# Kernel optimization log

Measured on AMD Instinct MI355X. Metric: run time of the kernel, lower is better.

Reference implementation:

```python
import jax, jax.numpy as jnp
import numpy as np

N_NODES = 100000
N_EDGES = 3200000
IN_F = 256
OUT_F = 128


def setup_inputs() -> dict:
    key = jax.random.key(0)
    k1, k2, k3, k4, k5, k6 = jax.random.split(key, 6)
    x = jax.random.normal(k1, (N_NODES, IN_F), dtype=jnp.float32)
    edge_row = jax.random.randint(k2, (N_EDGES,), 0, N_NODES, dtype=jnp.int32)
    edge_col = jax.random.randint(k3, (N_EDGES,), 0, N_NODES, dtype=jnp.int32)
    edge_val = jax.random.uniform(k4, (N_EDGES,), dtype=jnp.float32)
    # xavier_uniform with relu gain, as in reset_parameters
    gain = float(np.sqrt(2.0))
    bound = gain * float(np.sqrt(6.0 / (IN_F + OUT_F)))
    w = jax.random.uniform(k5, (IN_F, OUT_F), minval=-bound, maxval=bound, dtype=jnp.float32)
    std = 1.0 / float(np.sqrt(OUT_F))
    bias = jax.random.uniform(k6, (OUT_F,), minval=-std, maxval=std, dtype=jnp.float32)
    return {"x": x, "edge_row": edge_row, "edge_col": edge_col,
            "edge_val": edge_val, "w": w, "bias": bias}


def reference(x, edge_row, edge_col, edge_val, w, bias):
    # h = x @ w : dense feature transform [N, out]
    h = jnp.matmul(x, w)
    # spmm(adj, h): out[r] = sum_e adj_val[e] * h[c[e]] for edges e with row r
    msgs = edge_val[:, None] * h[edge_col]  # [E, out]
    agg = jax.ops.segment_sum(msgs, edge_row, num_segments=N_NODES)
    return agg + bias
```

## Files before the change

kernel.cpp:

```cpp
#include <hip/hip_runtime.h>
#include <hip/hip_bf16.h>

#define N_NODES 100000
#define N_EDGES 3200000
#define IN_F 256
#define OUT_F 128

#define RPB 128
#define NBIN 782
#define NBC  896
#define CHUNK 3572
#define GEMM_BLOCKS 782
#define BPTC 4
#define CAP 4608

typedef __attribute__((ext_vector_type(8))) short bf16x8;
typedef __attribute__((ext_vector_type(4))) float f32x4;

union U4BF { uint4 u; bf16x8 v; };

__device__ inline unsigned short f2bf(float f) {
    return __bfloat16_as_ushort(__float2bfloat16(f));
}
__device__ inline unsigned pk2(float a, float b) {
    unsigned la = __bfloat16_as_ushort(__float2bfloat16(a));
    unsigned lb = __bfloat16_as_ushort(__float2bfloat16(b));
    return la | (lb << 16);
}

__global__ __launch_bounds__(256) void conv_w_kernel(
    const float* __restrict__ w, uint4* __restrict__ wbfF)
{
    int tid = blockIdx.x * 256 + threadIdx.x;
    int ks = tid >> 9;
    int fn = (tid >> 6) & 7;
    int l  = tid & 63;
    int c  = fn * 16 + (l & 15);
    int k0 = ks * 32 + (l >> 4) * 8;
    const float* wp = w + (size_t)k0 * OUT_F + c;
    uint4 u;
    u.x = pk2(wp[0 * OUT_F], wp[1 * OUT_F]);
    u.y = pk2(wp[2 * OUT_F], wp[3 * OUT_F]);
    u.z = pk2(wp[4 * OUT_F], wp[5 * OUT_F]);
    u.w = pk2(wp[6 * OUT_F], wp[7 * OUT_F]);
    wbfF[tid] = u;
}

__global__ __launch_bounds__(256) void gemm_hist_kernel(
    const float* __restrict__ x, const uint4* __restrict__ wbfF,
    unsigned short* __restrict__ h,
    const int* __restrict__ erow, int* __restrict__ cntmat)
{
    __shared__ __align__(16) char smem[65536];
    const int t = threadIdx.x;

    if (blockIdx.x < GEMM_BLOCKS) {
        uint4* bsh = (uint4*)smem;
        const int lane = t & 63;
        const int wid  = t >> 6;
        const int brow = blockIdx.x * 128;
        const int ln   = lane & 15;
        const int kb   = lane >> 4;

#pragma unroll
        for (int i = 0; i < 16; ++i) bsh[i * 256 + t] = wbfF[i * 256 + t];

        int r0 = brow + wid * 32 + ln;
        int r1 = r0 + 16;
        const float* a0p = x + (size_t)(r0 < N_NODES ? r0 : N_NODES - 1) * IN_F;
        const float* a1p = x + (size_t)(r1 < N_NODES ? r1 : N_NODES - 1) * IN_F;

        f32x4 acc[2][8] = {};
        __syncthreads();

#pragma unroll
        for (int ks = 0; ks < 8; ++ks) {
            const int k = ks * 32 + kb * 8;
            U4BF a0, a1;
            {
                float4 p = *(const float4*)(a0p + k);
                float4 q = *(const float4*)(a0p + k + 4);
                a0.u.x = pk2(p.x, p.y); a0.u.y = pk2(p.z, p.w);
                a0.u.z = pk2(q.x, q.y); a0.u.w = pk2(q.z, q.w);
            }
            {
                float4 p = *(const float4*)(a1p + k);
                float4 q = *(const float4*)(a1p + k + 4);
                a1.u.x = pk2(p.x, p.y); a1.u.y = pk2(p.z, p.w);
                a1.u.z = pk2(q.x, q.y); a1.u.w = pk2(q.z, q.w);
            }
            U4BF b[8];
#pragma unroll
            for (int fn = 0; fn < 8; ++fn)
                b[fn].u = bsh[(ks * 8 + fn) * 64 + lane];
#pragma unroll
            for (int fn = 0; fn < 8; ++fn) {
                acc[0][fn] = __builtin_amdgcn_mfma_f32_16x16x32_bf16(
                    a0.v, b[fn].v, acc[0][fn], 0, 0, 0);
                acc[1][fn] = __builtin_amdgcn_mfma_f32_16x16x32_bf16(
                    a1.v, b[fn].v, acc[1][fn], 0, 0, 0);
            }
        }

#pragma unroll
        for (int fm = 0; fm < 2; ++fm) {
#pragma unroll
            for (int r = 0; r < 4; ++r) {
                int grow = brow + wid * 32 + fm * 16 + (lane >> 4) * 4 + r;
                if (grow < N_NODES) {
                    unsigned short* dst = h + (size_t)grow * OUT_F + ln;
#pragma unroll
                    for (int fn = 0; fn < 8; ++fn)
                        dst[fn * 16] = f2bf(acc[fm][fn][r]);
                }
            }
        }
    } else {
        int* lhist = (int*)smem;
        const int b = blockIdx.x - GEMM_BLOCKS;
        for (int i = t; i < NBIN; i += 256) lhist[i] = 0;
        __syncthreads();

        const int base = b * CHUNK;
        const int end  = min(base + CHUNK, N_EDGES);
        for (int i = base + t * 4; i < end; i += 1024) {
            int4 r = *(const int4*)(erow + i);
            atomicAdd(&lhist[r.x >> 7], 1);
            atomicAdd(&lhist[r.y >> 7], 1);
            atomicAdd(&lhist[r.z >> 7], 1);
            atomicAdd(&lhist[r.w >> 7], 1);
        }
        __syncthreads();

        int* dst = cntmat + (size_t)b * NBIN;
        for (int j = t; j < NBIN; j += 256) dst[j] = lhist[j];
    }
}

__global__ __launch_bounds__(256) void pass_b_kernel(
    const int* __restrict__ cntmat, int* __restrict__ blockbase,
    int* __restrict__ tot)
{
    __shared__ int sh[256];
    const int t = threadIdx.x;
    const int j = blockIdx.x;
    int c[4];
    int ps = 0;
#pragma unroll
    for (int i = 0; i < 4; ++i) {
        int bb = 4 * t + i;
        c[i] = (bb < NBC) ? cntmat[(size_t)bb * NBIN + j] : 0;
        ps += c[i];
    }
    sh[t] = ps;
    __syncthreads();
    for (int off = 1; off < 256; off <<= 1) {
        int add = (t >= off) ? sh[t - off] : 0;
        __syncthreads();
        sh[t] += add;
        __syncthreads();
    }
    int excl = sh[t] - ps;
#pragma unroll
    for (int i = 0; i < 4; ++i) {
        int bb = 4 * t + i;
        if (bb < NBC) { blockbase[(size_t)bb * NBIN + j] = excl; excl += c[i]; }
    }
    if (t == 255) tot[j] = sh[255];
}

__global__ __launch_bounds__(512) void pass_b2_kernel(
    const int* __restrict__ tot, int* __restrict__ bucket_base)
{
    __shared__ int sh[512];
    const int t = threadIdx.x;
    const int i0 = 2 * t, i1 = 2 * t + 1;
    int v0 = (i0 < NBIN) ? tot[i0] : 0;
    int v1 = (i1 < NBIN) ? tot[i1] : 0;
    int ps = v0 + v1;
    sh[t] = ps;
    __syncthreads();
    for (int off = 1; off < 512; off <<= 1) {
        int add = (t >= off) ? sh[t - off] : 0;
        __syncthreads();
        sh[t] += add;
        __syncthreads();
    }
    int excl = sh[t] - ps;
    if (i0 <= NBIN) bucket_base[i0] = excl;
    if (i1 <= NBIN) bucket_base[i1] = excl + v0;
}

__global__ __launch_bounds__(256) void pass_c_kernel(
    const int* __restrict__ erow, const int* __restrict__ ecol,
    const float* __restrict__ eval_, const int* __restrict__ cntmat,
    const int* __restrict__ blockbase, const int* __restrict__ bucket_base,
    int2* __restrict__ tmp)
{
    __shared__ int2 skv[CHUNK];
    __shared__ unsigned short sbin[CHUNK];
    __shared__ int  cur[NBIN];
    __shared__ int  sdel[NBIN];
    __shared__ int  sscan[256];

    const int t = threadIdx.x;
    const int b = blockIdx.x;

    int c[BPTC];
    int ps = 0;
#pragma unroll
    for (int i = 0; i < BPTC; ++i) {
        int bin = t * BPTC + i;
        c[i] = (bin < NBIN) ? cntmat[(size_t)b * NBIN + bin] : 0;
        ps += c[i];
    }
    sscan[t] = ps;
    __syncthreads();
    for (int off = 1; off < 256; off <<= 1) {
        int add = (t >= off) ? sscan[t - off] : 0;
        __syncthreads();
        sscan[t] += add;
        __syncthreads();
    }
    int excl = sscan[t] - ps;
#pragma unroll
    for (int i = 0; i < BPTC; ++i) {
        int bin = t * BPTC + i;
        if (bin < NBIN) {
            cur[bin]  = excl;
            sdel[bin] = bucket_base[bin] + blockbase[(size_t)b * NBIN + bin] - excl;
            excl += c[i];
        }
    }
    __syncthreads();

    const int base = b * CHUNK;
    const int end  = min(base + CHUNK, N_EDGES);
    for (int i = base + t * 4; i < end; i += 1024) {
        int4   r = *(const int4*)(erow + i);
        int4   cc = *(const int4*)(ecol + i);
        float4 v = *(const float4*)(eval_ + i);
        int bin, pos;
        bin = r.x >> 7; pos = atomicAdd(&cur[bin], 1);
        skv[pos] = make_int2(cc.x | ((r.x & 127) << 17), __float_as_int(v.x));
        sbin[pos] = (unsigned short)bin;
        bin = r.y >> 7; pos = atomicAdd(&cur[bin], 1);
        skv[pos] = make_int2(cc.y | ((r.y & 127) << 17), __float_as_int(v.y));
        sbin[pos] = (unsigned short)bin;
        bin = r.z >> 7; pos = atomicAdd(&cur[bin], 1);
        skv[pos] = make_int2(cc.z | ((r.z & 127) << 17), __float_as_int(v.z));
        sbin[pos] = (unsigned short)bin;
        bin = r.w >> 7; pos = atomicAdd(&cur[bin], 1);
        skv[pos] = make_int2(cc.w | ((r.w & 127) << 17), __float_as_int(v.w));
        sbin[pos] = (unsigned short)bin;
    }
    __syncthreads();

    const int n = end - base;
    for (int i = t; i < n; i += 256) {
        int2 kv = skv[i];
        tmp[sdel[sbin[i]] + i] = kv;
    }
}

__global__ __launch_bounds__(512) void fused_da_kernel(
    const int2* __restrict__ tmp, const int* __restrict__ bucket_base,
    const unsigned* __restrict__ h2, const float* __restrict__ bias,
    float* __restrict__ out)
{
    __shared__ int2 skv[CAP];
    __shared__ int  srow[RPB];
    __shared__ int  scnt[RPB];
    __shared__ int  cursor[RPB];

    const int t    = threadIdx.x;
    const int lane = t & 63;
    const int w    = t >> 6;
    const int j    = blockIdx.x;
    const int base = bucket_base[j];
    int n = bucket_base[j + 1] - base;
    if (n > CAP) n = CAP;

    if (t < RPB) cursor[t] = 0;
    __syncthreads();
    for (int i = t; i < n; i += 512)
        atomicAdd(&cursor[tmp[base + i].x >> 17], 1);
    __syncthreads();
    if (t < RPB) { scnt[t] = cursor[t]; srow[t] = cursor[t]; }
    __syncthreads();
    for (int off = 1; off < RPB; off <<= 1) {
        int add = (t >= off && t < RPB) ? srow[t - off] : 0;
        __syncthreads();
        if (t < RPB) srow[t] += add;
        __syncthreads();
    }
    if (t < RPB) { int ex = srow[t] - scnt[t]; srow[t] = ex; cursor[t] = ex; }
    __syncthreads();

    for (int i = t; i < n; i += 512) {
        int2 p = tmp[base + i];
        int rl = p.x >> 17;
        int pos = atomicAdd(&cursor[rl], 1);
        skv[pos] = make_int2(p.x & 0x1FFFF, p.y);
    }
    __syncthreads();

    const unsigned* hb = h2 + lane;
#pragma unroll 1
    for (int rr = w * 16; rr < w * 16 + 16; ++rr) {
        int gr = j * RPB + rr;
        if (gr >= N_NODES) break;
        int s = srow[rr];
        int end = s + scnt[rr];
        float ax = 0.f, ay = 0.f;

        int e = s;
        for (; e + 7 < end; e += 8) {
            int2 p0 = skv[e];
            int2 p1 = skv[e + 1];
            int2 p2 = skv[e + 2];
            int2 p3 = skv[e + 3];
            int2 p4 = skv[e + 4];
            int2 p5 = skv[e + 5];
            int2 p6 = skv[e + 6];
            int2 p7 = skv[e + 7];
            unsigned u0 = hb[(size_t)p0.x << 6];
            unsigned u1 = hb[(size_t)p1.x << 6];
            unsigned u2 = hb[(size_t)p2.x << 6];
            unsigned u3 = hb[(size_t)p3.x << 6];
            unsigned u4 = hb[(size_t)p4.x << 6];
            unsigned u5 = hb[(size_t)p5.x << 6];
            unsigned u6 = hb[(size_t)p6.x << 6];
            unsigned u7 = hb[(size_t)p7.x << 6];
            float v0 = __int_as_float(p0.y), v1 = __int_as_float(p1.y);
            float v2 = __int_as_float(p2.y), v3 = __int_as_float(p3.y);
            float v4 = __int_as_float(p4.y), v5 = __int_as_float(p5.y);
            float v6 = __int_as_float(p6.y), v7 = __int_as_float(p7.y);
            ax = fmaf(v0, __uint_as_float(u0 << 16), ax);
            ay = fmaf(v0, __uint_as_float(u0 & 0xFFFF0000u), ay);
            ax = fmaf(v1, __uint_as_float(u1 << 16), ax);
            ay = fmaf(v1, __uint_as_float(u1 & 0xFFFF0000u), ay);
            ax = fmaf(v2, __uint_as_float(u2 << 16), ax);
            ay = fmaf(v2, __uint_as_float(u2 & 0xFFFF0000u), ay);
            ax = fmaf(v3, __uint_as_float(u3 << 16), ax);
            ay = fmaf(v3, __uint_as_float(u3 & 0xFFFF0000u), ay);
            ax = fmaf(v4, __uint_as_float(u4 << 16), ax);
            ay = fmaf(v4, __uint_as_float(u4 & 0xFFFF0000u), ay);
            ax = fmaf(v5, __uint_as_float(u5 << 16), ax);
            ay = fmaf(v5, __uint_as_float(u5 & 0xFFFF0000u), ay);
            ax = fmaf(v6, __uint_as_float(u6 << 16), ax);
            ay = fmaf(v6, __uint_as_float(u6 & 0xFFFF0000u), ay);
            ax = fmaf(v7, __uint_as_float(u7 << 16), ax);
            ay = fmaf(v7, __uint_as_float(u7 & 0xFFFF0000u), ay);
        }
        for (; e < end; ++e) {
            int2 p0 = skv[e];
            unsigned u0 = hb[(size_t)p0.x << 6];
            float v0 = __int_as_float(p0.y);
            ax = fmaf(v0, __uint_as_float(u0 << 16), ax);
            ay = fmaf(v0, __uint_as_float(u0 & 0xFFFF0000u), ay);
        }

        float2 bb = *(const float2*)(bias + lane * 2);
        *(float2*)(out + (size_t)gr * OUT_F + lane * 2) =
            make_float2(ax + bb.x, ay + bb.y);
    }
}

extern "C" void kernel_launch(void* const* d_in, const int* in_sizes, int n_in,
                              void* d_out, int out_size, void* d_ws, size_t ws_size,
                              hipStream_t stream)
{
    const float* x     = (const float*)d_in[0];
    const int*   erow  = (const int*)d_in[1];
    const int*   ecol  = (const int*)d_in[2];
    const float* eval_ = (const float*)d_in[3];
    const float* w     = (const float*)d_in[4];
    const float* bias  = (const float*)d_in[5];
    float*       out   = (float*)d_out;

    char* ws = (char*)d_ws;
    unsigned short* h           = (unsigned short*)(ws);
    int2*           tmp         = (int2*)(ws + 25600000);
    int*            cntmat      = (int*)(ws + 51200000);
    int*            blockbase   = (int*)(ws + 54002688);
    int*            tot         = (int*)(ws + 56805376);
    int*            bucket_base = (int*)(ws + 56812000);
    uint4*          wbfF        = (uint4*)(ws + 56816000);

    hipLaunchKernelGGL(conv_w_kernel, dim3(16), dim3(256), 0, stream, w, wbfF);

    hipLaunchKernelGGL(gemm_hist_kernel, dim3(GEMM_BLOCKS + NBC), dim3(256), 0, stream,
                       x, wbfF, h, erow, cntmat);

    hipLaunchKernelGGL(pass_b_kernel, dim3(NBIN), dim3(256), 0, stream,
                       cntmat, blockbase, tot);
    hipLaunchKernelGGL(pass_b2_kernel, dim3(1), dim3(512), 0, stream, tot, bucket_base);

    hipLaunchKernelGGL(pass_c_kernel, dim3(NBC), dim3(256), 0, stream,
                       erow, ecol, eval_, cntmat, blockbase, bucket_base, tmp);

    hipLaunchKernelGGL(fused_da_kernel, dim3(NBIN), dim3(512), 0, stream,
                       tmp, bucket_base, (const unsigned*)h, bias, out);
}
```

Measured before the change: 197.5 us.

## Regroup kernels: fuse weight conversion with histogram, overlap GEMM with scatter pass

Weight bf16 conversion now shares a launch with the edge histogram, and the dense GEMM now shares a launch with the bucket scatter (pass C) rather than with the histogram. This removes one kernel launch and lets the heavier scatter overlap the GEMM. Separately, the aggregation kernel caches each bucket's edges in shared memory on the first read and sorts 16-bit indices instead of rewriting int2 pairs, so the global tmp array is read once instead of twice. The cost is an extra indirection through shared memory in the inner gather loop and more shared memory per block.

After: 236.4 us. 1.2x slower.

```diff
diff --git a/kernel.cpp b/kernel.cpp
--- a/kernel.cpp
+++ b/kernel.cpp
@@ -11,6 +11,7 @@
 #define NBC  896
 #define CHUNK 3572
 #define GEMM_BLOCKS 782
+#define CONV_BLOCKS 16
 #define BPTC 4
 #define CAP 4608
 
@@ -28,28 +29,109 @@
     return la | (lb << 16);
 }
 
-__global__ __launch_bounds__(256) void conv_w_kernel(
-    const float* __restrict__ w, uint4* __restrict__ wbfF)
-{
-    int tid = blockIdx.x * 256 + threadIdx.x;
-    int ks = tid >> 9;
-    int fn = (tid >> 6) & 7;
-    int l  = tid & 63;
-    int c  = fn * 16 + (l & 15);
-    int k0 = ks * 32 + (l >> 4) * 8;
-    const float* wp = w + (size_t)k0 * OUT_F + c;
-    uint4 u;
-    u.x = pk2(wp[0 * OUT_F], wp[1 * OUT_F]);
-    u.y = pk2(wp[2 * OUT_F], wp[3 * OUT_F]);
-    u.z = pk2(wp[4 * OUT_F], wp[5 * OUT_F]);
-    u.w = pk2(wp[6 * OUT_F], wp[7 * OUT_F]);
-    wbfF[tid] = u;
-}
-
-__global__ __launch_bounds__(256) void gemm_hist_kernel(
+__global__ __launch_bounds__(256) void conv_hist_kernel(
+    const float* __restrict__ w, uint4* __restrict__ wbfF,
+    const int* __restrict__ erow, int* __restrict__ cntmat)
+{
+    __shared__ int lhist[NBIN];
+    const int t = threadIdx.x;
+
+    if (blockIdx.x < CONV_BLOCKS) {
+        int tid = blockIdx.x * 256 + t;
+        int ks = tid >> 9;
+        int fn = (tid >> 6) & 7;
+        int l  = tid & 63;
+        int c  = fn * 16 + (l & 15);
+        int k0 = ks * 32 + (l >> 4) * 8;
+        const float* wp = w + (size_t)k0 * OUT_F + c;
+        uint4 u;
+        u.x = pk2(wp[0 * OUT_F], wp[1 * OUT_F]);
+        u.y = pk2(wp[2 * OUT_F], wp[3 * OUT_F]);
+        u.z = pk2(wp[4 * OUT_F], wp[5 * OUT_F]);
+        u.w = pk2(wp[6 * OUT_F], wp[7 * OUT_F]);
+        wbfF[tid] = u;
+    } else {
+        const int b = blockIdx.x - CONV_BLOCKS;
+        for (int i = t; i < NBIN; i += 256) lhist[i] = 0;
+        __syncthreads();
+
+        const int base = b * CHUNK;
+        const int end  = min(base + CHUNK, N_EDGES);
+        for (int i = base + t * 4; i < end; i += 1024) {
+            int4 r = *(const int4*)(erow + i);
+            atomicAdd(&lhist[r.x >> 7], 1);
+            atomicAdd(&lhist[r.y >> 7], 1);
+            atomicAdd(&lhist[r.z >> 7], 1);
+            atomicAdd(&lhist[r.w >> 7], 1);
+        }
+        __syncthreads();
+
+        int* dst = cntmat + (size_t)b * NBIN;
+        for (int j = t; j < NBIN; j += 256) dst[j] = lhist[j];
+    }
+}
+
+__global__ __launch_bounds__(256) void pass_b_kernel(
+    const int* __restrict__ cntmat, int* __restrict__ blockbase,
+    int* __restrict__ tot)
+{
+    __shared__ int sh[256];
+    const int t = threadIdx.x;
+    const int j = blockIdx.x;
+    int c[4];
+    int ps = 0;
+#pragma unroll
+    for (int i = 0; i < 4; ++i) {
+        int bb = 4 * t + i;
+        c[i] = (bb < NBC) ? cntmat[(size_t)bb * NBIN + j] : 0;
+        ps += c[i];
+    }
+    sh[t] = ps;
+    __syncthreads();
+    for (int off = 1; off < 256; off <<= 1) {
+        int add = (t >= off) ? sh[t - off] : 0;
+        __syncthreads();
+        sh[t] += add;
+        __syncthreads();
+    }
+    int excl = sh[t] - ps;
+#pragma unroll
+    for (int i = 0; i < 4; ++i) {
+        int bb = 4 * t + i;
+        if (bb < NBC) { blockbase[(size_t)bb * NBIN + j] = excl; excl += c[i]; }
+    }
+    if (t == 255) tot[j] = sh[255];
+}
+
+__global__ __launch_bounds__(512) void pass_b2_kernel(
+    const int* __restrict__ tot, int* __restrict__ bucket_base)
+{
+    __shared__ int sh[512];
+    const int t = threadIdx.x;
+    const int i0 = 2 * t, i1 = 2 * t + 1;
+    int v0 = (i0 < NBIN) ? tot[i0] : 0;
+    int v1 = (i1 < NBIN) ? tot[i1] : 0;
+    int ps = v0 + v1;
+    sh[t] = ps;
+    __syncthreads();
+    for (int off = 1; off < 512; off <<= 1) {
+        int add = (t >= off) ? sh[t - off] : 0;
+        __syncthreads();
+        sh[t] += add;
+        __syncthreads();
+    }
+    int excl = sh[t] - ps;
+    if (i0 <= NBIN) bucket_base[i0] = excl;
+    if (i1 <= NBIN) bucket_base[i1] = excl + v0;
+}
+
+__global__ __launch_bounds__(256) void gemm_passc_kernel(
     const float* __restrict__ x, const uint4* __restrict__ wbfF,
     unsigned short* __restrict__ h,
-    const int* __restrict__ erow, int* __restrict__ cntmat)
+    const int* __restrict__ erow, const int* __restrict__ ecol,
+    const float* __restrict__ eval_, const int* __restrict__ cntmat,
+    const int* __restrict__ blockbase, const int* __restrict__ bucket_base,
+    int2* __restrict__ tmp)
 {
     __shared__ __align__(16) char smem[65536];
     const int t = threadIdx.x;
@@ -116,150 +198,69 @@
             }
         }
     } else {
-        int* lhist = (int*)smem;
+        int2*           skv   = (int2*)(smem);
+        unsigned short* sbin  = (unsigned short*)(smem + 28576);
+        int*            cur   = (int*)(smem + 35720);
+        int*            sdel  = (int*)(smem + 38848);
+        int*            sscan = (int*)(smem + 41976);
+
         const int b = blockIdx.x - GEMM_BLOCKS;
-        for (int i = t; i < NBIN; i += 256) lhist[i] = 0;
+
+        int c[BPTC];
+        int ps = 0;
+#pragma unroll
+        for (int i = 0; i < BPTC; ++i) {
+            int bin = t * BPTC + i;
+            c[i] = (bin < NBIN) ? cntmat[(size_t)b * NBIN + bin] : 0;
+            ps += c[i];
+        }
+        sscan[t] = ps;
+        __syncthreads();
+        for (int off = 1; off < 256; off <<= 1) {
+            int add = (t >= off) ? sscan[t - off] : 0;
+            __syncthreads();
+            sscan[t] += add;
+            __syncthreads();
+        }
+        int excl = sscan[t] - ps;
+#pragma unroll
+        for (int i = 0; i < BPTC; ++i) {
+            int bin = t * BPTC + i;
+            if (bin < NBIN) {
+                cur[bin]  = excl;
+                sdel[bin] = bucket_base[bin] + blockbase[(size_t)b * NBIN + bin] - excl;
+                excl += c[i];
+            }
+        }
         __syncthreads();
 
         const int base = b * CHUNK;
         const int end  = min(base + CHUNK, N_EDGES);
         for (int i = base + t * 4; i < end; i += 1024) {
-            int4 r = *(const int4*)(erow + i);
-            atomicAdd(&lhist[r.x >> 7], 1);
-            atomicAdd(&lhist[r.y >> 7], 1);
-            atomicAdd(&lhist[r.z >> 7], 1);
-            atomicAdd(&lhist[r.w >> 7], 1);
-        }
-        __syncthreads();
-
-        int* dst = cntmat + (size_t)b * NBIN;
-        for (int j = t; j < NBIN; j += 256) dst[j] = lhist[j];
-    }
-}
-
-__global__ __launch_bounds__(256) void pass_b_kernel(
-    const int* __restrict__ cntmat, int* __restrict__ blockbase,
-    int* __restrict__ tot)
-{
-    __shared__ int sh[256];
-    const int t = threadIdx.x;
-    const int j = blockIdx.x;
-    int c[4];
-    int ps = 0;
-#pragma unroll
-    for (int i = 0; i < 4; ++i) {
-        int bb = 4 * t + i;
-        c[i] = (bb < NBC) ? cntmat[(size_t)bb * NBIN + j] : 0;
-        ps += c[i];
-    }
-    sh[t] = ps;
-    __syncthreads();
-    for (int off = 1; off < 256; off <<= 1) {
-        int add = (t >= off) ? sh[t - off] : 0;
-        __syncthreads();
-        sh[t] += add;
-        __syncthreads();
-    }
-    int excl = sh[t] - ps;
-#pragma unroll
-    for (int i = 0; i < 4; ++i) {
-        int bb = 4 * t + i;
-        if (bb < NBC) { blockbase[(size_t)bb * NBIN + j] = excl; excl += c[i]; }
-    }
-    if (t == 255) tot[j] = sh[255];
-}
-
-__global__ __launch_bounds__(512) void pass_b2_kernel(
-    const int* __restrict__ tot, int* __restrict__ bucket_base)
-{
-    __shared__ int sh[512];
-    const int t = threadIdx.x;
-    const int i0 = 2 * t, i1 = 2 * t + 1;
-    int v0 = (i0 < NBIN) ? tot[i0] : 0;
-    int v1 = (i1 < NBIN) ? tot[i1] : 0;
-    int ps = v0 + v1;
-    sh[t] = ps;
-    __syncthreads();
-    for (int off = 1; off < 512; off <<= 1) {
-        int add = (t >= off) ? sh[t - off] : 0;
-        __syncthreads();
-        sh[t] += add;
-        __syncthreads();
-    }
-    int excl = sh[t] - ps;
-    if (i0 <= NBIN) bucket_base[i0] = excl;
-    if (i1 <= NBIN) bucket_base[i1] = excl + v0;
-}
-
-__global__ __launch_bounds__(256) void pass_c_kernel(
-    const int* __restrict__ erow, const int* __restrict__ ecol,
-    const float* __restrict__ eval_, const int* __restrict__ cntmat,
-    const int* __restrict__ blockbase, const int* __restrict__ bucket_base,
-    int2* __restrict__ tmp)
-{
-    __shared__ int2 skv[CHUNK];
-    __shared__ unsigned short sbin[CHUNK];
-    __shared__ int  cur[NBIN];
-    __shared__ int  sdel[NBIN];
-    __shared__ int  sscan[256];
-
-    const int t = threadIdx.x;
-    const int b = blockIdx.x;
-
-    int c[BPTC];
-    int ps = 0;
-#pragma unroll
-    for (int i = 0; i < BPTC; ++i) {
-        int bin = t * BPTC + i;
-        c[i] = (bin < NBIN) ? cntmat[(size_t)b * NBIN + bin] : 0;
-        ps += c[i];
-    }
-    sscan[t] = ps;
-    __syncthreads();
-    for (int off = 1; off < 256; off <<= 1) {
-        int add = (t >= off) ? sscan[t - off] : 0;
-        __syncthreads();
-        sscan[t] += add;
-        __syncthreads();
-    }
-    int excl = sscan[t] - ps;
-#pragma unroll
-    for (int i = 0; i < BPTC; ++i) {
-        int bin = t * BPTC + i;
-        if (bin < NBIN) {
-            cur[bin]  = excl;
-            sdel[bin] = bucket_base[bin] + blockbase[(size_t)b * NBIN + bin] - excl;
-            excl += c[i];
-        }
-    }
-    __syncthreads();
-
-    const int base = b * CHUNK;
-    const int end  = min(base + CHUNK, N_EDGES);
-    for (int i = base + t * 4; i < end; i += 1024) {
-        int4   r = *(const int4*)(erow + i);
-        int4   cc = *(const int4*)(ecol + i);
-        float4 v = *(const float4*)(eval_ + i);
-        int bin, pos;
-        bin = r.x >> 7; pos = atomicAdd(&cur[bin], 1);
-        skv[pos] = make_int2(cc.x | ((r.x & 127) << 17), __float_as_int(v.x));
-        sbin[pos] = (unsigned short)bin;
-        bin = r.y >> 7; pos = atomicAdd(&cur[bin], 1);
-        skv[pos] = make_int2(cc.y | ((r.y & 127) << 17), __float_as_int(v.y));
-        sbin[pos] = (unsigned short)bin;
-        bin = r.z >> 7; pos = atomicAdd(&cur[bin], 1);
-        skv[pos] = make_int2(cc.z | ((r.z & 127) << 17), __float_as_int(v.z));
-        sbin[pos] = (unsigned short)bin;
-        bin = r.w >> 7; pos = atomicAdd(&cur[bin], 1);
-        skv[pos] = make_int2(cc.w | ((r.w & 127) << 17), __float_as_int(v.w));
-        sbin[pos] = (unsigned short)bin;
-    }
-    __syncthreads();
-
-    const int n = end - base;
-    for (int i = t; i < n; i += 256) {
-        int2 kv = skv[i];
-        tmp[sdel[sbin[i]] + i] = kv;
+            int4   r = *(const int4*)(erow + i);
+            int4   cc = *(const int4*)(ecol + i);
+            float4 v = *(const float4*)(eval_ + i);
+            int bin, pos;
+            bin = r.x >> 7; pos = atomicAdd(&cur[bin], 1);
+            skv[pos] = make_int2(cc.x | ((r.x & 127) << 17), __float_as_int(v.x));
+            sbin[pos] = (unsigned short)bin;
+            bin = r.y >> 7; pos = atomicAdd(&cur[bin], 1);
+            skv[pos] = make_int2(cc.y | ((r.y & 127) << 17), __float_as_int(v.y));
+            sbin[pos] = (unsigned short)bin;
+            bin = r.z >> 7; pos = atomicAdd(&cur[bin], 1);
+            skv[pos] = make_int2(cc.z | ((r.z & 127) << 17), __float_as_int(v.z));
+            sbin[pos] = (unsigned short)bin;
+            bin = r.w >> 7; pos = atomicAdd(&cur[bin], 1);
+            skv[pos] = make_int2(cc.w | ((r.w & 127) << 17), __float_as_int(v.w));
+            sbin[pos] = (unsigned short)bin;
+        }
+        __syncthreads();
+
+        const int n = end - base;
+        for (int i = t; i < n; i += 256) {
+            int2 kv = skv[i];
+            tmp[sdel[sbin[i]] + i] = kv;
+        }
     }
 }
 
@@ -269,6 +270,7 @@
     float* __restrict__ out)
 {
     __shared__ int2 skv[CAP];
+    __shared__ unsigned short sidx[CAP];
     __shared__ int  srow[RPB];
     __shared__ int  scnt[RPB];
     __shared__ int  cursor[RPB];
@@ -283,9 +285,13 @@
 
     if (t < RPB) cursor[t] = 0;
     __syncthreads();
-    for (int i = t; i < n; i += 512)
-        atomicAdd(&cursor[tmp[base + i].x >> 17], 1);
-    __syncthreads();
+    for (int i = t; i < n; i += 512) {
+        int2 p = tmp[base + i];
+        skv[i] = p;
+        atomicAdd(&cursor[p.x >> 17], 1);
+    }
+    __syncthreads();
+
     if (t < RPB) { scnt[t] = cursor[t]; srow[t] = cursor[t]; }
     __syncthreads();
     for (int off = 1; off < RPB; off <<= 1) {
@@ -298,10 +304,9 @@
     __syncthreads();
 
     for (int i = t; i < n; i += 512) {
-        int2 p = tmp[base + i];
-        int rl = p.x >> 17;
+        int rl = skv[i].x >> 17;
         int pos = atomicAdd(&cursor[rl], 1);
-        skv[pos] = make_int2(p.x & 0x1FFFF, p.y);
+        sidx[pos] = (unsigned short)i;
     }
     __syncthreads();
 
@@ -316,22 +321,22 @@
 
         int e = s;
         for (; e + 7 < end; e += 8) {
-            int2 p0 = skv[e];
-            int2 p1 = skv[e + 1];
-            int2 p2 = skv[e + 2];
-            int2 p3 = skv[e + 3];
-            int2 p4 = skv[e + 4];
-            int2 p5 = skv[e + 5];
-            int2 p6 = skv[e + 6];
-            int2 p7 = skv[e + 7];
-            unsigned u0 = hb[(size_t)p0.x << 6];
-            unsigned u1 = hb[(size_t)p1.x << 6];
-            unsigned u2 = hb[(size_t)p2.x << 6];
-            unsigned u3 = hb[(size_t)p3.x << 6];
-            unsigned u4 = hb[(size_t)p4.x << 6];
-            unsigned u5 = hb[(size_t)p5.x << 6];
-            unsigned u6 = hb[(size_t)p6.x << 6];
-            unsigned u7 = hb[(size_t)p7.x << 6];
+            int2 p0 = skv[sidx[e]];
+            int2 p1 = skv[sidx[e + 1]];
+            int2 p2 = skv[sidx[e + 2]];
+            int2 p3 = skv[sidx[e + 3]];
+            int2 p4 = skv[sidx[e + 4]];
+            int2 p5 = skv[sidx[e + 5]];
+            int2 p6 = skv[sidx[e + 6]];
+            int2 p7 = skv[sidx[e + 7]];
+            unsigned u0 = hb[(size_t)(p0.x & 0x1FFFF) << 6];
+            unsigned u1 = hb[(size_t)(p1.x & 0x1FFFF) << 6];
+            unsigned u2 = hb[(size_t)(p2.x & 0x1FFFF) << 6];
+            unsigned u3 = hb[(size_t)(p3.x & 0x1FFFF) << 6];
+            unsigned u4 = hb[(size_t)(p4.x & 0x1FFFF) << 6];
+            unsigned u5 = hb[(size_t)(p5.x & 0x1FFFF) << 6];
+            unsigned u6 = hb[(size_t)(p6.x & 0x1FFFF) << 6];
+            unsigned u7 = hb[(size_t)(p7.x & 0x1FFFF) << 6];
             float v0 = __int_as_float(p0.y), v1 = __int_as_float(p1.y);
             float v2 = __int_as_float(p2.y), v3 = __int_as_float(p3.y);
             float v4 = __int_as_float(p4.y), v5 = __int_as_float(p5.y);
@@ -354,8 +359,8 @@
             ay = fmaf(v7, __uint_as_float(u7 & 0xFFFF0000u), ay);
         }
         for (; e < end; ++e) {
-            int2 p0 = skv[e];
-            unsigned u0 = hb[(size_t)p0.x << 6];
+            int2 p0 = skv[sidx[e]];
+            unsigned u0 = hb[(size_t)(p0.x & 0x1FFFF) << 6];
             float v0 = __int_as_float(p0.y);
             ax = fmaf(v0, __uint_as_float(u0 << 16), ax);
             ay = fmaf(v0, __uint_as_float(u0 & 0xFFFF0000u), ay);
@@ -388,17 +393,16 @@
     int*            bucket_base = (int*)(ws + 56812000);
     uint4*          wbfF        = (uint4*)(ws + 56816000);
 
-    hipLaunchKernelGGL(conv_w_kernel, dim3(16), dim3(256), 0, stream, w, wbfF);
-
-    hipLaunchKernelGGL(gemm_hist_kernel, dim3(GEMM_BLOCKS + NBC), dim3(256), 0, stream,
-                       x, wbfF, h, erow, cntmat);
+    hipLaunchKernelGGL(conv_hist_kernel, dim3(CONV_BLOCKS + NBC), dim3(256), 0, stream,
+                       w, wbfF, erow, cntmat);
 
     hipLaunchKernelGGL(pass_b_kernel, dim3(NBIN), dim3(256), 0, stream,
                        cntmat, blockbase, tot);
     hipLaunchKernelGGL(pass_b2_kernel, dim3(1), dim3(512), 0, stream, tot, bucket_base);
 
-    hipLaunchKernelGGL(pass_c_kernel, dim3(NBC), dim3(256), 0, stream,
-                       erow, ecol, eval_, cntmat, blockbase, bucket_base, tmp);
+    hipLaunchKernelGGL(gemm_passc_kernel, dim3(GEMM_BLOCKS + NBC), dim3(256), 0, stream,
+                       x, wbfF, h, erow, ecol, eval_, cntmat, blockbase,
+                       bucket_base, tmp);
 
     hipLaunchKernelGGL(fused_da_kernel, dim3(NBIN), dim3(512), 0, stream,
                        tmp, bucket_base, (const unsigned*)h, bias, out);
```

## Co-schedule GEMM with edge scatter pass instead of with histogram

Applied to the files above, without the earlier changes.

Moves the weight conversion into the histogram kernel and pairs the dense GEMM blocks with the heavier pass_c scatter blocks in one launch, so the GEMM overlaps the bucket scatter rather than the light histogram. The intent is to hide the costlier scatter pass behind GEMM compute and drop one kernel launch. The shared-memory carve-up for the scatter path is now manual offsets within the 64KB buffer.

New measurement: 191.6 us. 1.03x faster.

```diff
diff --git a/kernel.cpp b/kernel.cpp
--- a/kernel.cpp
+++ b/kernel.cpp
@@ -11,6 +11,7 @@
 #define NBC  896
 #define CHUNK 3572
 #define GEMM_BLOCKS 782
+#define CONV_BLOCKS 16
 #define BPTC 4
 #define CAP 4608
 
@@ -28,28 +29,109 @@
     return la | (lb << 16);
 }
 
-__global__ __launch_bounds__(256) void conv_w_kernel(
-    const float* __restrict__ w, uint4* __restrict__ wbfF)
-{
-    int tid = blockIdx.x * 256 + threadIdx.x;
-    int ks = tid >> 9;
-    int fn = (tid >> 6) & 7;
-    int l  = tid & 63;
-    int c  = fn * 16 + (l & 15);
-    int k0 = ks * 32 + (l >> 4) * 8;
-    const float* wp = w + (size_t)k0 * OUT_F + c;
-    uint4 u;
-    u.x = pk2(wp[0 * OUT_F], wp[1 * OUT_F]);
-    u.y = pk2(wp[2 * OUT_F], wp[3 * OUT_F]);
-    u.z = pk2(wp[4 * OUT_F], wp[5 * OUT_F]);
-    u.w = pk2(wp[6 * OUT_F], wp[7 * OUT_F]);
-    wbfF[tid] = u;
-}
-
-__global__ __launch_bounds__(256) void gemm_hist_kernel(
+__global__ __launch_bounds__(256) void conv_hist_kernel(
+    const float* __restrict__ w, uint4* __restrict__ wbfF,
+    const int* __restrict__ erow, int* __restrict__ cntmat)
+{
+    __shared__ int lhist[NBIN];
+    const int t = threadIdx.x;
+
+    if (blockIdx.x < CONV_BLOCKS) {
+        int tid = blockIdx.x * 256 + t;
+        int ks = tid >> 9;
+        int fn = (tid >> 6) & 7;
+        int l  = tid & 63;
+        int c  = fn * 16 + (l & 15);
+        int k0 = ks * 32 + (l >> 4) * 8;
+        const float* wp = w + (size_t)k0 * OUT_F + c;
+        uint4 u;
+        u.x = pk2(wp[0 * OUT_F], wp[1 * OUT_F]);
+        u.y = pk2(wp[2 * OUT_F], wp[3 * OUT_F]);
+        u.z = pk2(wp[4 * OUT_F], wp[5 * OUT_F]);
+        u.w = pk2(wp[6 * OUT_F], wp[7 * OUT_F]);
+        wbfF[tid] = u;
+    } else {
+        const int b = blockIdx.x - CONV_BLOCKS;
+        for (int i = t; i < NBIN; i += 256) lhist[i] = 0;
+        __syncthreads();
+
+        const int base = b * CHUNK;
+        const int end  = min(base + CHUNK, N_EDGES);
+        for (int i = base + t * 4; i < end; i += 1024) {
+            int4 r = *(const int4*)(erow + i);
+            atomicAdd(&lhist[r.x >> 7], 1);
+            atomicAdd(&lhist[r.y >> 7], 1);
+            atomicAdd(&lhist[r.z >> 7], 1);
+            atomicAdd(&lhist[r.w >> 7], 1);
+        }
+        __syncthreads();
+
+        int* dst = cntmat + (size_t)b * NBIN;
+        for (int j = t; j < NBIN; j += 256) dst[j] = lhist[j];
+    }
+}
+
+__global__ __launch_bounds__(256) void pass_b_kernel(
+    const int* __restrict__ cntmat, int* __restrict__ blockbase,
+    int* __restrict__ tot)
+{
+    __shared__ int sh[256];
+    const int t = threadIdx.x;
+    const int j = blockIdx.x;
+    int c[4];
+    int ps = 0;
+#pragma unroll
+    for (int i = 0; i < 4; ++i) {
+        int bb = 4 * t + i;
+        c[i] = (bb < NBC) ? cntmat[(size_t)bb * NBIN + j] : 0;
+        ps += c[i];
+    }
+    sh[t] = ps;
+    __syncthreads();
+    for (int off = 1; off < 256; off <<= 1) {
+        int add = (t >= off) ? sh[t - off] : 0;
+        __syncthreads();
+        sh[t] += add;
+        __syncthreads();
+    }
+    int excl = sh[t] - ps;
+#pragma unroll
+    for (int i = 0; i < 4; ++i) {
+        int bb = 4 * t + i;
+        if (bb < NBC) { blockbase[(size_t)bb * NBIN + j] = excl; excl += c[i]; }
+    }
+    if (t == 255) tot[j] = sh[255];
+}
+
+__global__ __launch_bounds__(512) void pass_b2_kernel(
+    const int* __restrict__ tot, int* __restrict__ bucket_base)
+{
+    __shared__ int sh[512];
+    const int t = threadIdx.x;
+    const int i0 = 2 * t, i1 = 2 * t + 1;
+    int v0 = (i0 < NBIN) ? tot[i0] : 0;
+    int v1 = (i1 < NBIN) ? tot[i1] : 0;
+    int ps = v0 + v1;
+    sh[t] = ps;
+    __syncthreads();
+    for (int off = 1; off < 512; off <<= 1) {
+        int add = (t >= off) ? sh[t - off] : 0;
+        __syncthreads();
+        sh[t] += add;
+        __syncthreads();
+    }
+    int excl = sh[t] - ps;
+    if (i0 <= NBIN) bucket_base[i0] = excl;
+    if (i1 <= NBIN) bucket_base[i1] = excl + v0;
+}
+
+__global__ __launch_bounds__(256) void gemm_passc_kernel(
     const float* __restrict__ x, const uint4* __restrict__ wbfF,
     unsigned short* __restrict__ h,
-    const int* __restrict__ erow, int* __restrict__ cntmat)
+    const int* __restrict__ erow, const int* __restrict__ ecol,
+    const float* __restrict__ eval_, const int* __restrict__ cntmat,
+    const int* __restrict__ blockbase, const int* __restrict__ bucket_base,
+    int2* __restrict__ tmp)
 {
     __shared__ __align__(16) char smem[65536];
     const int t = threadIdx.x;
@@ -116,150 +198,69 @@
             }
         }
     } else {
-        int* lhist = (int*)smem;
+        int2*           skv   = (int2*)(smem);
+        unsigned short* sbin  = (unsigned short*)(smem + 28576);
+        int*            cur   = (int*)(smem + 35720);
+        int*            sdel  = (int*)(smem + 38848);
+        int*            sscan = (int*)(smem + 41976);
+
         const int b = blockIdx.x - GEMM_BLOCKS;
-        for (int i = t; i < NBIN; i += 256) lhist[i] = 0;
+
+        int c[BPTC];
+        int ps = 0;
+#pragma unroll
+        for (int i = 0; i < BPTC; ++i) {
+            int bin = t * BPTC + i;
+            c[i] = (bin < NBIN) ? cntmat[(size_t)b * NBIN + bin] : 0;
+            ps += c[i];
+        }
+        sscan[t] = ps;
+        __syncthreads();
+        for (int off = 1; off < 256; off <<= 1) {
+            int add = (t >= off) ? sscan[t - off] : 0;
+            __syncthreads();
+            sscan[t] += add;
+            __syncthreads();
+        }
+        int excl = sscan[t] - ps;
+#pragma unroll
+        for (int i = 0; i < BPTC; ++i) {
+            int bin = t * BPTC + i;
+            if (bin < NBIN) {
+                cur[bin]  = excl;
+                sdel[bin] = bucket_base[bin] + blockbase[(size_t)b * NBIN + bin] - excl;
+                excl += c[i];
+            }
+        }
         __syncthreads();
 
         const int base = b * CHUNK;
         const int end  = min(base + CHUNK, N_EDGES);
         for (int i = base + t * 4; i < end; i += 1024) {
-            int4 r = *(const int4*)(erow + i);
-            atomicAdd(&lhist[r.x >> 7], 1);
-            atomicAdd(&lhist[r.y >> 7], 1);
-            atomicAdd(&lhist[r.z >> 7], 1);
-            atomicAdd(&lhist[r.w >> 7], 1);
-        }
-        __syncthreads();
-
-        int* dst = cntmat + (size_t)b * NBIN;
-        for (int j = t; j < NBIN; j += 256) dst[j] = lhist[j];
-    }
-}
-
-__global__ __launch_bounds__(256) void pass_b_kernel(
-    const int* __restrict__ cntmat, int* __restrict__ blockbase,
-    int* __restrict__ tot)
-{
-    __shared__ int sh[256];
-    const int t = threadIdx.x;
-    const int j = blockIdx.x;
-    int c[4];
-    int ps = 0;
-#pragma unroll
-    for (int i = 0; i < 4; ++i) {
-        int bb = 4 * t + i;
-        c[i] = (bb < NBC) ? cntmat[(size_t)bb * NBIN + j] : 0;
-        ps += c[i];
-    }
-    sh[t] = ps;
-    __syncthreads();
-    for (int off = 1; off < 256; off <<= 1) {
-        int add = (t >= off) ? sh[t - off] : 0;
-        __syncthreads();
-        sh[t] += add;
-        __syncthreads();
-    }
-    int excl = sh[t] - ps;
-#pragma unroll
-    for (int i = 0; i < 4; ++i) {
-        int bb = 4 * t + i;
-        if (bb < NBC) { blockbase[(size_t)bb * NBIN + j] = excl; excl += c[i]; }
-    }
-    if (t == 255) tot[j] = sh[255];
-}
-
-__global__ __launch_bounds__(512) void pass_b2_kernel(
-    const int* __restrict__ tot, int* __restrict__ bucket_base)
-{
-    __shared__ int sh[512];
-    const int t = threadIdx.x;
-    const int i0 = 2 * t, i1 = 2 * t + 1;
-    int v0 = (i0 < NBIN) ? tot[i0] : 0;
-    int v1 = (i1 < NBIN) ? tot[i1] : 0;
-    int ps = v0 + v1;
-    sh[t] = ps;
-    __syncthreads();
-    for (int off = 1; off < 512; off <<= 1) {
-        int add = (t >= off) ? sh[t - off] : 0;
-        __syncthreads();
-        sh[t] += add;
-        __syncthreads();
-    }
-    int excl = sh[t] - ps;
-    if (i0 <= NBIN) bucket_base[i0] = excl;
-    if (i1 <= NBIN) bucket_base[i1] = excl + v0;
-}
-
-__global__ __launch_bounds__(256) void pass_c_kernel(
-    const int* __restrict__ erow, const int* __restrict__ ecol,
-    const float* __restrict__ eval_, const int* __restrict__ cntmat,
-    const int* __restrict__ blockbase, const int* __restrict__ bucket_base,
-    int2* __restrict__ tmp)
-{
-    __shared__ int2 skv[CHUNK];
-    __shared__ unsigned short sbin[CHUNK];
-    __shared__ int  cur[NBIN];
-    __shared__ int  sdel[NBIN];
-    __shared__ int  sscan[256];
-
-    const int t = threadIdx.x;
-    const int b = blockIdx.x;
-
-    int c[BPTC];
-    int ps = 0;
-#pragma unroll
-    for (int i = 0; i < BPTC; ++i) {
-        int bin = t * BPTC + i;
-        c[i] = (bin < NBIN) ? cntmat[(size_t)b * NBIN + bin] : 0;
-        ps += c[i];
-    }
-    sscan[t] = ps;
-    __syncthreads();
-    for (int off = 1; off < 256; off <<= 1) {
-        int add = (t >= off) ? sscan[t - off] : 0;
-        __syncthreads();
-        sscan[t] += add;
-        __syncthreads();
-    }
-    int excl = sscan[t] - ps;
-#pragma unroll
-    for (int i = 0; i < BPTC; ++i) {
-        int bin = t * BPTC + i;
-        if (bin < NBIN) {
-            cur[bin]  = excl;
-            sdel[bin] = bucket_base[bin] + blockbase[(size_t)b * NBIN + bin] - excl;
-            excl += c[i];
-        }
-    }
-    __syncthreads();
-
-    const int base = b * CHUNK;
-    const int end  = min(base + CHUNK, N_EDGES);
-    for (int i = base + t * 4; i < end; i += 1024) {
-        int4   r = *(const int4*)(erow + i);
-        int4   cc = *(const int4*)(ecol + i);
-        float4 v = *(const float4*)(eval_ + i);
-        int bin, pos;
-        bin = r.x >> 7; pos = atomicAdd(&cur[bin], 1);
-        skv[pos] = make_int2(cc.x | ((r.x & 127) << 17), __float_as_int(v.x));
-        sbin[pos] = (unsigned short)bin;
-        bin = r.y >> 7; pos = atomicAdd(&cur[bin], 1);
-        skv[pos] = make_int2(cc.y | ((r.y & 127) << 17), __float_as_int(v.y));
-        sbin[pos] = (unsigned short)bin;
-        bin = r.z >> 7; pos = atomicAdd(&cur[bin], 1);
-        skv[pos] = make_int2(cc.z | ((r.z & 127) << 17), __float_as_int(v.z));
-        sbin[pos] = (unsigned short)bin;
-        bin = r.w >> 7; pos = atomicAdd(&cur[bin], 1);
-        skv[pos] = make_int2(cc.w | ((r.w & 127) << 17), __float_as_int(v.w));
-        sbin[pos] = (unsigned short)bin;
-    }
-    __syncthreads();
-
-    const int n = end - base;
-    for (int i = t; i < n; i += 256) {
-        int2 kv = skv[i];
-        tmp[sdel[sbin[i]] + i] = kv;
+            int4   r = *(const int4*)(erow + i);
+            int4   cc = *(const int4*)(ecol + i);
+            float4 v = *(const float4*)(eval_ + i);
+            int bin, pos;
+            bin = r.x >> 7; pos = atomicAdd(&cur[bin], 1);
+            skv[pos] = make_int2(cc.x | ((r.x & 127) << 17), __float_as_int(v.x));
+            sbin[pos] = (unsigned short)bin;
+            bin = r.y >> 7; pos = atomicAdd(&cur[bin], 1);
+            skv[pos] = make_int2(cc.y | ((r.y & 127) << 17), __float_as_int(v.y));
+            sbin[pos] = (unsigned short)bin;
+            bin = r.z >> 7; pos = atomicAdd(&cur[bin], 1);
+            skv[pos] = make_int2(cc.z | ((r.z & 127) << 17), __float_as_int(v.z));
+            sbin[pos] = (unsigned short)bin;
+            bin = r.w >> 7; pos = atomicAdd(&cur[bin], 1);
+            skv[pos] = make_int2(cc.w | ((r.w & 127) << 17), __float_as_int(v.w));
+            sbin[pos] = (unsigned short)bin;
+        }
+        __syncthreads();
+
+        const int n = end - base;
+        for (int i = t; i < n; i += 256) {
+            int2 kv = skv[i];
+            tmp[sdel[sbin[i]] + i] = kv;
+        }
     }
 }
 
@@ -388,17 +389,16 @@
     int*            bucket_base = (int*)(ws + 56812000);
     uint4*          wbfF        = (uint4*)(ws + 56816000);
 
-    hipLaunchKernelGGL(conv_w_kernel, dim3(16), dim3(256), 0, stream, w, wbfF);
-
-    hipLaunchKernelGGL(gemm_hist_kernel, dim3(GEMM_BLOCKS + NBC), dim3(256), 0, stream,
-                       x, wbfF, h, erow, cntmat);
+    hipLaunchKernelGGL(conv_hist_kernel, dim3(CONV_BLOCKS + NBC), dim3(256), 0, stream,
+                       w, wbfF, erow, cntmat);
 
     hipLaunchKernelGGL(pass_b_kernel, dim3(NBIN), dim3(256), 0, stream,
                        cntmat, blockbase, tot);
     hipLaunchKernelGGL(pass_b2_kernel, dim3(1), dim3(512), 0, stream, tot, bucket_base);
 
-    hipLaunchKernelGGL(pass_c_kernel, dim3(NBC), dim3(256), 0, stream,
-                       erow, ecol, eval_, cntmat, blockbase, bucket_base, tmp);
+    hipLaunchKernelGGL(gemm_passc_kernel, dim3(GEMM_BLOCKS + NBC), dim3(256), 0, stream,
+                       x, wbfF, h, erow, ecol, eval_, cntmat, blockbase,
+                       bucket_base, tmp);
 
     hipLaunchKernelGGL(fused_da_kernel, dim3(NBIN), dim3(512), 0, stream,
                        tmp, bucket_base, (const unsigned*)h, bias, out);
```
